# Kernel tuning notes

Measured on AMD Instinct MI355X. Metric: run time of the kernel, lower is better.

The kernel has to match this reference:

```python
import jax, jax.numpy as jnp
import numpy as np

NUM_HEADS = 8
MASK_RATE = 0.5


def setup_inputs() -> dict:
    key = jax.random.key(0)
    ks = jax.random.split(key, 6)
    B, N, C = 8, 1024, 256
    TABLE = 10
    att_embedding = jax.random.normal(ks[0], (B, N, C), dtype=jnp.float32)
    relation_position = jax.random.randint(ks[1], (B, N, N), 0, TABLE, dtype=jnp.int32)
    rel_len = jax.random.randint(ks[2], (B,), 0, 20, dtype=jnp.int32)
    W_qkv = jax.random.normal(ks[3], (C, 3 * C), dtype=jnp.float32) * (1.0 / np.sqrt(C))
    W_proj = jax.random.normal(ks[4], (C, C), dtype=jnp.float32) * (1.0 / np.sqrt(C))
    b_proj = jnp.zeros((C,), dtype=jnp.float32)
    bias_table = jax.random.normal(ks[5], (TABLE, NUM_HEADS), dtype=jnp.float32) * 0.02
    return {
        "att_embedding": att_embedding,
        "relation_position": relation_position,
        "rel_len": rel_len,
        "W_qkv": W_qkv,
        "W_proj": W_proj,
        "b_proj": b_proj,
        "bias_table": bias_table,
    }


def reference(att_embedding, relation_position, rel_len, W_qkv, W_proj, b_proj, bias_table):
    B, N, C = att_embedding.shape
    H = NUM_HEADS
    hd = C // H
    scale = hd ** -0.5

    # QKV projection (no bias): [B,N,3C] -> q,k,v each [B,H,N,hd]
    qkv = (att_embedding @ W_qkv).reshape(B, N, 3, H, hd)
    qkv = jnp.transpose(qkv, (2, 0, 3, 1, 4))
    q, k, v = qkv[0], qkv[1], qkv[2]

    # Attention scores [B,H,N,N]
    attn = jnp.einsum("bhnd,bhmd->bhnm", q, k) * scale

    # Relative position bias: gather [B,N,N,H] -> [B,H,N,N]
    pos_bias = jnp.transpose(bias_table[relation_position], (0, 3, 1, 2))

    # Mask bias: table row t gets -100 iff t > mask_len (mask_len+1 .. TABLE-1);
    # identical across heads -> compute as [B,1,N,N] instead of materializing [B,H,N,N].
    mask_len = (rel_len.astype(jnp.float32) * MASK_RATE).astype(jnp.int32)
    mask_bias = jnp.where(relation_position > mask_len[:, None, None], -100.0, 0.0)[:, None]

    attn = jax.nn.softmax(attn + pos_bias + mask_bias, axis=-1)

    # Weighted values -> [B,N,C] -> output projection
    x = jnp.einsum("bhnm,bhmd->bnhd", attn, v).reshape(B, N, C)
    x = x @ W_proj + b_proj
    return x
```

## Files before the change

kernel.cpp:

```cpp
#include <hip/hip_runtime.h>
#include <hip/hip_bf16.h>

typedef __bf16 bf16;
typedef __bf16 bf16x2 __attribute__((ext_vector_type(2)));
typedef __bf16 bf16x4 __attribute__((ext_vector_type(4)));
typedef __bf16 bf16x8 __attribute__((ext_vector_type(8)));
typedef float f32x4 __attribute__((ext_vector_type(4)));
typedef int i32x4 __attribute__((ext_vector_type(4)));

#define B_ 8
#define N_ 1024
#define C_ 256
#define H_ 8
#define C3_ 768
#define SCALE 0.17677669529663689f
#define FMAX 16.0f


__global__ __launch_bounds__(256) void gemm_qkv(
    const float* __restrict__ A, const float* __restrict__ Wqkv,
    const float* __restrict__ Wproj, const int* __restrict__ rel,
    bf16* __restrict__ q, bf16* __restrict__ kT, bf16* __restrict__ vT,
    bf16* __restrict__ Wp_tiled, unsigned char* __restrict__ rel8)
{
  __shared__ __align__(16) char sm[18432];

  int bb = blockIdx.x;
  int tid = threadIdx.x;

  if (bb >= 768) {
    if (bb < 2816) {
      long p = ((long)(bb - 768) * 256 + tid) * 16;
      i32x4 a = *reinterpret_cast<const i32x4*>(rel + p);
      i32x4 b2 = *reinterpret_cast<const i32x4*>(rel + p + 4);
      i32x4 c = *reinterpret_cast<const i32x4*>(rel + p + 8);
      i32x4 d = *reinterpret_cast<const i32x4*>(rel + p + 12);
      unsigned o0 = (unsigned)a[0] | ((unsigned)a[1] << 8) | ((unsigned)a[2] << 16) | ((unsigned)a[3] << 24);
      unsigned o1 = (unsigned)b2[0] | ((unsigned)b2[1] << 8) | ((unsigned)b2[2] << 16) | ((unsigned)b2[3] << 24);
      unsigned o2 = (unsigned)c[0] | ((unsigned)c[1] << 8) | ((unsigned)c[2] << 16) | ((unsigned)c[3] << 24);
      unsigned o3 = (unsigned)d[0] | ((unsigned)d[1] << 8) | ((unsigned)d[2] << 16) | ((unsigned)d[3] << 24);
      i32x4 ov = {(int)o0, (int)o1, (int)o2, (int)o3};
      *reinterpret_cast<i32x4*>(rel8 + p) = ov;
    } else {
      int p = (bb - 2816) * 256 + tid;
      int kk = p & 31;
      int n = (p >> 5) & 255;
      int kt = p >> 13;
      Wp_tiled[p] = (bf16)Wproj[(kt * 32 + kk) * C_ + n];
    }
    return;
  }

  bf16 (*As)[40] = (bf16(*)[40])(void*)sm;
  bf16 (*Bs)[40] = (bf16(*)[40])(void*)(sm + 5120);

  int wave = tid >> 6, lane = tid & 63, quad = lane >> 4, l16 = lane & 15;
  int x = bb & 127, y = bb >> 7;
  int m0 = x * 64, n0 = y * 128;
  int msub = (wave & 1) * 32, nsub = (wave >> 1) * 64;

  f32x4 acc[2][4] = {};

  int arow = tid >> 2, akc = (tid & 3) * 8;
  const float* aptr = A + (long)(m0 + arow) * C_ + akc;

  int bk = tid >> 3, bns = (tid & 7) * 16;
  int bcp = (((bk >> 3) ^ (tid & 3)) << 3) + (bk & 7);
  const float* wq = Wqkv + (long)bk * C3_ + n0 + bns;

  float4 a0 = *reinterpret_cast<const float4*>(aptr);
  float4 a1 = *reinterpret_cast<const float4*>(aptr + 4);
  float4 f0 = *reinterpret_cast<const float4*>(wq);
  float4 f1 = *reinterpret_cast<const float4*>(wq + 4);
  float4 f2 = *reinterpret_cast<const float4*>(wq + 8);
  float4 f3 = *reinterpret_cast<const float4*>(wq + 12);

  for (int kt = 0; kt < 8; ++kt) {
    __syncthreads();
    {
      bf16 at[8] = {(bf16)a0.x, (bf16)a0.y, (bf16)a0.z, (bf16)a0.w,
                    (bf16)a1.x, (bf16)a1.y, (bf16)a1.z, (bf16)a1.w};
      *reinterpret_cast<bf16x8*>(&As[arow][akc]) = *reinterpret_cast<bf16x8*>(at);
      float vv[16] = {f0.x, f0.y, f0.z, f0.w, f1.x, f1.y, f1.z, f1.w,
                      f2.x, f2.y, f2.z, f2.w, f3.x, f3.y, f3.z, f3.w};
#pragma unroll
      for (int i = 0; i < 16; ++i)
        Bs[bns + i][bcp] = (bf16)vv[i];
    }
    __syncthreads();

    if (kt < 7) {
      int kn = (kt + 1) * 32;
      a0 = *reinterpret_cast<const float4*>(aptr + kn);
      a1 = *reinterpret_cast<const float4*>(aptr + kn + 4);
      const float* wqn = wq + (long)kn * C3_;
      f0 = *reinterpret_cast<const float4*>(wqn);
      f1 = *reinterpret_cast<const float4*>(wqn + 4);
      f2 = *reinterpret_cast<const float4*>(wqn + 8);
      f3 = *reinterpret_cast<const float4*>(wqn + 12);
    }

    bf16x8 af[2], bfr[4];
#pragma unroll
    for (int mi = 0; mi < 2; ++mi)
      af[mi] = *reinterpret_cast<const bf16x8*>(&As[msub + mi * 16 + l16][quad * 8]);
#pragma unroll
    for (int ni = 0; ni < 4; ++ni)
      bfr[ni] = *reinterpret_cast<const bf16x8*>(
          &Bs[nsub + ni * 16 + l16][(quad ^ ni) << 3]);
#pragma unroll
    for (int mi = 0; mi < 2; ++mi)
#pragma unroll
      for (int ni = 0; ni < 4; ++ni)
        acc[mi][ni] = __builtin_amdgcn_mfma_f32_16x16x32_bf16(af[mi], bfr[ni], acc[mi][ni], 0, 0, 0);
  }

  __syncthreads();

  if (y < 4) {
    float mul = (y < 2) ? SCALE : 1.0f;
    bf16 (*Ep)[136] = (bf16(*)[136])(void*)sm;
#pragma unroll
    for (int mi = 0; mi < 2; ++mi)
#pragma unroll
      for (int ni = 0; ni < 4; ++ni)
#pragma unroll
        for (int r = 0; r < 4; ++r)
          Ep[msub + mi * 16 + quad * 4 + r][nsub + ni * 16 + l16] =
              (bf16)(acc[mi][ni][r] * mul);
    __syncthreads();
    int row = tid >> 2, seg = tid & 3;
    i32x4 w0 = *reinterpret_cast<const i32x4*>(&Ep[row][seg * 32]);
    i32x4 w1 = *reinterpret_cast<const i32x4*>(&Ep[row][seg * 32 + 8]);
    i32x4 w2 = *reinterpret_cast<const i32x4*>(&Ep[row][seg * 32 + 16]);
    i32x4 w3 = *reinterpret_cast<const i32x4*>(&Ep[row][seg * 32 + 24]);
    bf16* dst;
    if (y < 2) {
      dst = q + (long)(m0 + row) * 256 + n0 + seg * 32;
    } else {
      int c = n0 - 256 + seg * 32;
      int h = c >> 5;
      int gr = m0 + row, b = gr >> 10, n = gr & 1023;
      dst = kT + (((long)(b * H_ + h)) * N_ + n) * 32;
    }
    *reinterpret_cast<i32x4*>(dst) = w0;
    *reinterpret_cast<i32x4*>(dst + 8) = w1;
    *reinterpret_cast<i32x4*>(dst + 16) = w2;
    *reinterpret_cast<i32x4*>(dst + 24) = w3;
  } else {
    bf16 (*Vls)[72] = (bf16(*)[72])(void*)sm;
#pragma unroll
    for (int mi = 0; mi < 2; ++mi)
#pragma unroll
      for (int ni = 0; ni < 4; ++ni)
#pragma unroll
        for (int r = 0; r < 4; ++r) {
          int nn = msub + mi * 16 + quad * 4 + r;
          int np = (nn & ~31) | ((nn & 12) << 1) | (nn & 3) | (((nn >> 4) & 1) << 2);
          Vls[nsub + ni * 16 + l16][np] = (bf16)acc[mi][ni][r];
        }
    __syncthreads();
    int c = tid >> 1, nseg = (tid & 1) * 32;
    i32x4 w0 = *reinterpret_cast<const i32x4*>(&Vls[c][nseg]);
    i32x4 w1 = *reinterpret_cast<const i32x4*>(&Vls[c][nseg + 8]);
    i32x4 w2 = *reinterpret_cast<const i32x4*>(&Vls[c][nseg + 16]);
    i32x4 w3 = *reinterpret_cast<const i32x4*>(&Vls[c][nseg + 24]);
    int gb = m0 >> 10, mn = m0 & 1023;
    bf16* dst = vT + ((long)(gb * C_ + (n0 - 512) + c)) * N_ + mn + nseg;
    *reinterpret_cast<i32x4*>(dst) = w0;
    *reinterpret_cast<i32x4*>(dst + 8) = w1;
    *reinterpret_cast<i32x4*>(dst + 16) = w2;
    *reinterpret_cast<i32x4*>(dst + 24) = w3;
  }
}

__global__ __launch_bounds__(512) void flash_attn(
    const bf16* __restrict__ q, const bf16* __restrict__ kT,
    const bf16* __restrict__ vT, const unsigned char* __restrict__ rel8,
    const int* __restrict__ rel_len, const float* __restrict__ btab,
    const bf16* __restrict__ Wp_tiled, const float* __restrict__ bias,
    float* __restrict__ out)
{
  __shared__ __align__(16) char smem[74240];
  char* const KB0 = smem;
  char* const VB0 = smem + 32768;
  char* const RB0 = smem + 65536;
  float* const ebtl = (float*)(smem + 73728);

  int tid = threadIdx.x;
  int h = tid >> 6, lane = tid & 63, quad = lane >> 4, l16 = lane & 15;

  int wg = blockIdx.y * 64 + blockIdx.x;
  int swz = (wg & 7) * 64 + (wg >> 3);
  int b = swz >> 6, i0 = (swz & 63) * 16;
  long bN = (long)b * N_;

  int mask_len = (int)((float)rel_len[b] * 0.5f);
  if (tid < 80) {
    int t = tid >> 3, hh = tid & 7;
    ebtl[hh * 16 + t] = __expf(btab[t * H_ + hh] + (t > mask_len ? -100.f : 0.f) - FMAX);
  }

  bf16x8 qf = *reinterpret_cast<const bf16x8*>(
      q + (bN + i0 + l16) * 256 + h * 32 + quad * 8);

  __syncthreads();

  int l = lane;
  int sxc = (((l & 3) ^ ((l >> 3) & 3)) << 4);
  int kc0 = (l >> 2) * 64 + sxc;
  int vc0 = (h * 32 + (l >> 2)) * 2048 + sxc;
  int rc0 = (l >> 3) * 1024 + (l & 7) * 4;

  const char* kTb = (const char*)kT + ((long)(b * 8 + h) << 16);
  const char* vTb = (const char*)vT + (long)b * 524288;
  const char* rb8 = (const char*)rel8 + (bN + i0) * 1024;

  int swq = ((quad ^ ((l16 >> 1) & 3)) << 4);
  int kr = h * 2048 + l16 * 64 + swq;
  int rr = h * 512 + l16 * 32 + quad * 4;

#define KB(i) (KB0 + (i) * 16384)
#define VB(i) (VB0 + (i) * 16384)
#define RB(i) (RB0 + (i) * 4096)

#define GLD16(G, L) __builtin_amdgcn_global_load_lds(                         \
    (const __attribute__((address_space(1))) void*)(G),                       \
    (__attribute__((address_space(3))) void*)(L), 16, 0, 0)
#define GLD4(G, L) __builtin_amdgcn_global_load_lds(                          \
    (const __attribute__((address_space(1))) void*)(G),                       \
    (__attribute__((address_space(3))) void*)(L), 4, 0, 0)

#define GATH(G, RV0, RV1) do {                                                \
    _Pragma("unroll")                                                         \
    for (int e = 0; e < 4; ++e) {                                             \
      G[e]     = ebtl[h * 16 + (int)((RV0 >> (8 * e)) & 255u)];               \
      G[4 + e] = ebtl[h * 16 + (int)((RV1 >> (8 * e)) & 255u)];               \
    }                                                                         \
  } while (0)

#define COMP(K0, K1, V0, V1, G) do {                                          \
    f32x4 z = {};                                                             \
    f32x4 s0 = __builtin_amdgcn_mfma_f32_16x16x32_bf16(K0, qf, z, 0, 0, 0);   \
    f32x4 s1 = __builtin_amdgcn_mfma_f32_16x16x32_bf16(K1, qf, z, 0, 0, 0);   \
    bf16x8 pa;                                                                \
    _Pragma("unroll")                                                         \
    for (int e = 0; e < 4; ++e) {                                             \
      float p0 = __expf(s0[e]) * G[e];                                        \
      float p1 = __expf(s1[e]) * G[4 + e];                                    \
      l_acc += p0 + p1;                                                       \
      pa[e] = (bf16)p0;                                                       \
      pa[4 + e] = (bf16)p1;                                                   \
    }                                                                         \
    oacc[0] = __builtin_amdgcn_mfma_f32_16x16x32_bf16(pa, V0, oacc[0], 0, 0, 0); \
    oacc[1] = __builtin_amdgcn_mfma_f32_16x16x32_bf16(pa, V1, oacc[1], 0, 0, 0); \
  } while (0)

#define TILE(T_, KVR, KVW, GC, GN) do {                                       \
    int tn_ = ((T_) + 1) & 31, tr_ = ((T_) + 2) & 31;                         \
    GLD16(kTb + tn_ * 2048 + kc0,        KB(KVW) + h * 2048);                 \
    GLD16(kTb + tn_ * 2048 + kc0 + 1024, KB(KVW) + h * 2048 + 1024);          \
    GLD16(vTb + tn_ * 64 + vc0,          VB(KVW) + h * 2048);                 \
    GLD16(vTb + tn_ * 64 + vc0 + 32768,  VB(KVW) + h * 2048 + 1024);          \
    GLD4(rb8 + tr_ * 32 + rc0,           RB(KVR) + h * 512);                  \
    GLD4(rb8 + tr_ * 32 + rc0 + 8192,    RB(KVR) + h * 512 + 256);            \
    asm volatile("s_waitcnt vmcnt(6)" ::: "memory");                          \
    bf16x8 kf0 = *(const bf16x8*)(KB(KVR) + kr);                              \
    bf16x8 kf1 = *(const bf16x8*)(KB(KVR) + kr + 1024);                       \
    bf16x8 vf0 = *(const bf16x8*)(VB(KVR) + kr);                              \
    bf16x8 vf1 = *(const bf16x8*)(VB(KVR) + kr + 1024);                       \
    unsigned rv0 = *(const unsigned*)(RB(KVW) + rr);                          \
    unsigned rv1 = *(const unsigned*)(RB(KVW) + rr + 16);                     \
    GATH(GN, rv0, rv1);                                                       \
    COMP(kf0, kf1, vf0, vf1, GC);                                             \
  } while (0)

  f32x4 oacc[2] = {};
  float l_acc = 0.f;
  float gA[8], gB[8];

  GLD16(kTb + kc0,        KB(0) + h * 2048);
  GLD16(kTb + kc0 + 1024, KB(0) + h * 2048 + 1024);
  GLD16(vTb + vc0,          VB(0) + h * 2048);
  GLD16(vTb + vc0 + 32768,  VB(0) + h * 2048 + 1024);
  GLD4(rb8 + rc0,             RB(0) + h * 512);
  GLD4(rb8 + rc0 + 8192,      RB(0) + h * 512 + 256);
  GLD4(rb8 + 32 + rc0,        RB(1) + h * 512);
  GLD4(rb8 + 32 + rc0 + 8192, RB(1) + h * 512 + 256);
  asm volatile("s_waitcnt vmcnt(0)" ::: "memory");
  {
    unsigned rv0 = *(const unsigned*)(RB(0) + rr);
    unsigned rv1 = *(const unsigned*)(RB(0) + rr + 16);
    GATH(gA, rv0, rv1);
  }

#pragma unroll 1
  for (int t = 0; t < 32; t += 2) {
    TILE(t + 0, 0, 1, gA, gB);
    TILE(t + 1, 1, 0, gB, gA);
  }
#undef TILE
#undef COMP
#undef GATH
#undef GLD16
#undef GLD4
#undef KB
#undef VB
#undef RB

  asm volatile("s_waitcnt vmcnt(0)" ::: "memory");
  __syncthreads();

  float lsum = l_acc;
  lsum += __shfl_xor(lsum, 16);
  lsum += __shfl_xor(lsum, 32);
  float inv = 1.f / lsum;

  bf16 (*attL)[264] = (bf16(*)[264])(void*)smem;
#pragma unroll
  for (int r = 0; r < 4; ++r) {
    float invr = __shfl(inv, quad * 4 + r);
    attL[quad * 4 + r][h * 32 + l16] = (bf16)(oacc[0][r] * invr);
    attL[quad * 4 + r][h * 32 + 16 + l16] = (bf16)(oacc[1][r] * invr);
  }
  __syncthreads();

  f32x4 pacc[2] = {};
  const bf16* wp = Wp_tiled + ((h * 32 + l16) * 32 + quad * 8);
#pragma unroll
  for (int kt = 0; kt < 8; ++kt) {
    bf16x8 afr = *reinterpret_cast<const bf16x8*>(&attL[l16][kt * 32 + quad * 8]);
    bf16x8 b0 = *reinterpret_cast<const bf16x8*>(wp + kt * 8192);
    bf16x8 b1 = *reinterpret_cast<const bf16x8*>(wp + kt * 8192 + 512);
    pacc[0] = __builtin_amdgcn_mfma_f32_16x16x32_bf16(afr, b0, pacc[0], 0, 0, 0);
    pacc[1] = __builtin_amdgcn_mfma_f32_16x16x32_bf16(afr, b1, pacc[1], 0, 0, 0);
  }
  float bi0 = bias[h * 32 + l16];
  float bi1 = bias[h * 32 + 16 + l16];
#pragma unroll
  for (int r = 0; r < 4; ++r) {
    long rowoff = (bN + i0 + quad * 4 + r) * C_ + h * 32;
    out[rowoff + l16] = pacc[0][r] + bi0;
    out[rowoff + 16 + l16] = pacc[1][r] + bi1;
  }
}

extern "C" void kernel_launch(void* const* d_in, const int* in_sizes, int n_in,
                              void* d_out, int out_size, void* d_ws, size_t ws_size,
                              hipStream_t stream) {
  const float* X     = (const float*)d_in[0];
  const int*   rel   = (const int*)d_in[1];
  const int*   rlen  = (const int*)d_in[2];
  const float* Wqkv  = (const float*)d_in[3];
  const float* Wproj = (const float*)d_in[4];
  const float* bproj = (const float*)d_in[5];
  const float* btab  = (const float*)d_in[6];
  float* out = (float*)d_out;

  char* ws = (char*)d_ws;
  bf16* Wp_tiled = (bf16*)(ws + 393216);
  bf16* q  = (bf16*)(ws + 524288);
  bf16* kT = (bf16*)(ws + 524288 + 4194304);
  bf16* vT = (bf16*)(ws + 524288 + 2 * 4194304);
  unsigned char* rel8 = (unsigned char*)(ws + 13107200);

  gemm_qkv<<<dim3(3072), 256, 0, stream>>>(X, Wqkv, Wproj, rel,
                                           q, kT, vT, Wp_tiled, rel8);
  flash_attn<<<dim3(N_ / 16, B_), 512, 0, stream>>>(
      q, kT, vT, rel8, rlen, btab, Wp_tiled, bproj, out);
}
```

Measured before the change: 141.0 us.

## Process 32 query rows per block to reuse K/V tiles across two row groups

Each flash-attention workgroup now handles 32 query rows (two 16-row MFMA groups) instead of 16, so every K/V tile staged in LDS feeds twice as many MFMAs. The goal is to halve global K/V traffic per query. The grid halves to 256 blocks, the rel8 buffer doubles and its loads widen to 16 bytes, and register pressure rises. Fewer blocks may leave CUs underused on a 256-CU part.

Measured after the change: 131.3 us (median of 2 runs). 6.9% less time.

```diff
diff --git a/kernel.cpp b/kernel.cpp
--- a/kernel.cpp
+++ b/kernel.cpp
@@ -181,18 +181,18 @@
     const bf16* __restrict__ Wp_tiled, const float* __restrict__ bias,
     float* __restrict__ out)
 {
-  __shared__ __align__(16) char smem[74240];
+  __shared__ __align__(16) char smem[82432];
   char* const KB0 = smem;
   char* const VB0 = smem + 32768;
   char* const RB0 = smem + 65536;
-  float* const ebtl = (float*)(smem + 73728);
+  float* const ebtl = (float*)(smem + 81920);
 
   int tid = threadIdx.x;
   int h = tid >> 6, lane = tid & 63, quad = lane >> 4, l16 = lane & 15;
 
-  int wg = blockIdx.y * 64 + blockIdx.x;
-  int swz = (wg & 7) * 64 + (wg >> 3);
-  int b = swz >> 6, i0 = (swz & 63) * 16;
+  int wg = blockIdx.y * 32 + blockIdx.x;
+  int swz = (wg & 7) * 32 + (wg >> 3);
+  int b = swz >> 5, i0 = (swz & 31) * 32;
   long bN = (long)b * N_;
 
   int mask_len = (int)((float)rel_len[b] * 0.5f);
@@ -201,8 +201,10 @@
     ebtl[hh * 16 + t] = __expf(btab[t * H_ + hh] + (t > mask_len ? -100.f : 0.f) - FMAX);
   }
 
-  bf16x8 qf = *reinterpret_cast<const bf16x8*>(
+  bf16x8 qfA = *reinterpret_cast<const bf16x8*>(
       q + (bN + i0 + l16) * 256 + h * 32 + quad * 8);
+  bf16x8 qfB = *reinterpret_cast<const bf16x8*>(
+      q + (bN + i0 + 16 + l16) * 256 + h * 32 + quad * 8);
 
   __syncthreads();
 
@@ -210,7 +212,7 @@
   int sxc = (((l & 3) ^ ((l >> 3) & 3)) << 4);
   int kc0 = (l >> 2) * 64 + sxc;
   int vc0 = (h * 32 + (l >> 2)) * 2048 + sxc;
-  int rc0 = (l >> 3) * 1024 + (l & 7) * 4;
+  int rc0 = (l >> 1) * 1024 + (l & 1) * 16;
 
   const char* kTb = (const char*)kT + ((long)(b * 8 + h) << 16);
   const char* vTb = (const char*)vT + (long)b * 524288;
@@ -218,42 +220,48 @@
 
   int swq = ((quad ^ ((l16 >> 1) & 3)) << 4);
   int kr = h * 2048 + l16 * 64 + swq;
-  int rr = h * 512 + l16 * 32 + quad * 4;
+  int rr = h * 1024 + l16 * 32 + quad * 4;
 
 #define KB(i) (KB0 + (i) * 16384)
 #define VB(i) (VB0 + (i) * 16384)
-#define RB(i) (RB0 + (i) * 4096)
+#define RB(i) (RB0 + (i) * 8192)
 
 #define GLD16(G, L) __builtin_amdgcn_global_load_lds(                         \
     (const __attribute__((address_space(1))) void*)(G),                       \
     (__attribute__((address_space(3))) void*)(L), 16, 0, 0)
-#define GLD4(G, L) __builtin_amdgcn_global_load_lds(                          \
-    (const __attribute__((address_space(1))) void*)(G),                       \
-    (__attribute__((address_space(3))) void*)(L), 4, 0, 0)
-
-#define GATH(G, RV0, RV1) do {                                                \
+
+#define GATH(G, RV0, RV1, RV2, RV3) do {                                      \
     _Pragma("unroll")                                                         \
     for (int e = 0; e < 4; ++e) {                                             \
-      G[e]     = ebtl[h * 16 + (int)((RV0 >> (8 * e)) & 255u)];               \
-      G[4 + e] = ebtl[h * 16 + (int)((RV1 >> (8 * e)) & 255u)];               \
+      G[e]      = ebtl[h * 16 + (int)((RV0 >> (8 * e)) & 255u)];              \
+      G[4 + e]  = ebtl[h * 16 + (int)((RV1 >> (8 * e)) & 255u)];              \
+      G[8 + e]  = ebtl[h * 16 + (int)((RV2 >> (8 * e)) & 255u)];              \
+      G[12 + e] = ebtl[h * 16 + (int)((RV3 >> (8 * e)) & 255u)];              \
     }                                                                         \
   } while (0)
 
 #define COMP(K0, K1, V0, V1, G) do {                                          \
     f32x4 z = {};                                                             \
-    f32x4 s0 = __builtin_amdgcn_mfma_f32_16x16x32_bf16(K0, qf, z, 0, 0, 0);   \
-    f32x4 s1 = __builtin_amdgcn_mfma_f32_16x16x32_bf16(K1, qf, z, 0, 0, 0);   \
-    bf16x8 pa;                                                                \
+    f32x4 s0A = __builtin_amdgcn_mfma_f32_16x16x32_bf16(K0, qfA, z, 0, 0, 0); \
+    f32x4 s1A = __builtin_amdgcn_mfma_f32_16x16x32_bf16(K1, qfA, z, 0, 0, 0); \
+    f32x4 s0B = __builtin_amdgcn_mfma_f32_16x16x32_bf16(K0, qfB, z, 0, 0, 0); \
+    f32x4 s1B = __builtin_amdgcn_mfma_f32_16x16x32_bf16(K1, qfB, z, 0, 0, 0); \
+    bf16x8 paA, paB;                                                          \
     _Pragma("unroll")                                                         \
     for (int e = 0; e < 4; ++e) {                                             \
-      float p0 = __expf(s0[e]) * G[e];                                        \
-      float p1 = __expf(s1[e]) * G[4 + e];                                    \
-      l_acc += p0 + p1;                                                       \
-      pa[e] = (bf16)p0;                                                       \
-      pa[4 + e] = (bf16)p1;                                                   \
+      float pA0 = __expf(s0A[e]) * G[e];                                      \
+      float pA1 = __expf(s1A[e]) * G[4 + e];                                  \
+      float pB0 = __expf(s0B[e]) * G[8 + e];                                  \
+      float pB1 = __expf(s1B[e]) * G[12 + e];                                 \
+      l_accA += pA0 + pA1;                                                    \
+      l_accB += pB0 + pB1;                                                    \
+      paA[e] = (bf16)pA0; paA[4 + e] = (bf16)pA1;                             \
+      paB[e] = (bf16)pB0; paB[4 + e] = (bf16)pB1;                             \
     }                                                                         \
-    oacc[0] = __builtin_amdgcn_mfma_f32_16x16x32_bf16(pa, V0, oacc[0], 0, 0, 0); \
-    oacc[1] = __builtin_amdgcn_mfma_f32_16x16x32_bf16(pa, V1, oacc[1], 0, 0, 0); \
+    oA0 = __builtin_amdgcn_mfma_f32_16x16x32_bf16(paA, V0, oA0, 0, 0, 0);     \
+    oA1 = __builtin_amdgcn_mfma_f32_16x16x32_bf16(paA, V1, oA1, 0, 0, 0);     \
+    oB0 = __builtin_amdgcn_mfma_f32_16x16x32_bf16(paB, V0, oB0, 0, 0, 0);     \
+    oB1 = __builtin_amdgcn_mfma_f32_16x16x32_bf16(paB, V1, oB1, 0, 0, 0);     \
   } while (0)
 
 #define TILE(T_, KVR, KVW, GC, GN) do {                                       \
@@ -262,36 +270,37 @@
     GLD16(kTb + tn_ * 2048 + kc0 + 1024, KB(KVW) + h * 2048 + 1024);          \
     GLD16(vTb + tn_ * 64 + vc0,          VB(KVW) + h * 2048);                 \
     GLD16(vTb + tn_ * 64 + vc0 + 32768,  VB(KVW) + h * 2048 + 1024);          \
-    GLD4(rb8 + tr_ * 32 + rc0,           RB(KVR) + h * 512);                  \
-    GLD4(rb8 + tr_ * 32 + rc0 + 8192,    RB(KVR) + h * 512 + 256);            \
-    asm volatile("s_waitcnt vmcnt(6)" ::: "memory");                          \
+    GLD16(rb8 + tr_ * 32 + rc0,          RB(KVR) + h * 1024);                 \
+    asm volatile("s_waitcnt vmcnt(5)" ::: "memory");                          \
     bf16x8 kf0 = *(const bf16x8*)(KB(KVR) + kr);                              \
     bf16x8 kf1 = *(const bf16x8*)(KB(KVR) + kr + 1024);                       \
     bf16x8 vf0 = *(const bf16x8*)(VB(KVR) + kr);                              \
     bf16x8 vf1 = *(const bf16x8*)(VB(KVR) + kr + 1024);                       \
     unsigned rv0 = *(const unsigned*)(RB(KVW) + rr);                          \
     unsigned rv1 = *(const unsigned*)(RB(KVW) + rr + 16);                     \
-    GATH(GN, rv0, rv1);                                                       \
+    unsigned rv2 = *(const unsigned*)(RB(KVW) + rr + 512);                    \
+    unsigned rv3 = *(const unsigned*)(RB(KVW) + rr + 528);                    \
+    GATH(GN, rv0, rv1, rv2, rv3);                                             \
     COMP(kf0, kf1, vf0, vf1, GC);                                             \
   } while (0)
 
-  f32x4 oacc[2] = {};
-  float l_acc = 0.f;
-  float gA[8], gB[8];
+  f32x4 oA0 = {}, oA1 = {}, oB0 = {}, oB1 = {};
+  float l_accA = 0.f, l_accB = 0.f;
+  float gA[16], gB[16];
 
   GLD16(kTb + kc0,        KB(0) + h * 2048);
   GLD16(kTb + kc0 + 1024, KB(0) + h * 2048 + 1024);
   GLD16(vTb + vc0,          VB(0) + h * 2048);
   GLD16(vTb + vc0 + 32768,  VB(0) + h * 2048 + 1024);
-  GLD4(rb8 + rc0,             RB(0) + h * 512);
-  GLD4(rb8 + rc0 + 8192,      RB(0) + h * 512 + 256);
-  GLD4(rb8 + 32 + rc0,        RB(1) + h * 512);
-  GLD4(rb8 + 32 + rc0 + 8192, RB(1) + h * 512 + 256);
+  GLD16(rb8 + rc0,        RB(0) + h * 1024);
+  GLD16(rb8 + 32 + rc0,   RB(1) + h * 1024);
   asm volatile("s_waitcnt vmcnt(0)" ::: "memory");
   {
     unsigned rv0 = *(const unsigned*)(RB(0) + rr);
     unsigned rv1 = *(const unsigned*)(RB(0) + rr + 16);
-    GATH(gA, rv0, rv1);
+    unsigned rv2 = *(const unsigned*)(RB(0) + rr + 512);
+    unsigned rv3 = *(const unsigned*)(RB(0) + rr + 528);
+    GATH(gA, rv0, rv1, rv2, rv3);
   }
 
 #pragma unroll 1
@@ -303,7 +312,6 @@
 #undef COMP
 #undef GATH
 #undef GLD16
-#undef GLD4
 #undef KB
 #undef VB
 #undef RB
@@ -311,37 +319,50 @@
   asm volatile("s_waitcnt vmcnt(0)" ::: "memory");
   __syncthreads();
 
-  float lsum = l_acc;
-  lsum += __shfl_xor(lsum, 16);
-  lsum += __shfl_xor(lsum, 32);
-  float inv = 1.f / lsum;
+  float lsumA = l_accA;
+  lsumA += __shfl_xor(lsumA, 16);
+  lsumA += __shfl_xor(lsumA, 32);
+  float invA = 1.f / lsumA;
+  float lsumB = l_accB;
+  lsumB += __shfl_xor(lsumB, 16);
+  lsumB += __shfl_xor(lsumB, 32);
+  float invB = 1.f / lsumB;
 
   bf16 (*attL)[264] = (bf16(*)[264])(void*)smem;
 #pragma unroll
   for (int r = 0; r < 4; ++r) {
-    float invr = __shfl(inv, quad * 4 + r);
-    attL[quad * 4 + r][h * 32 + l16] = (bf16)(oacc[0][r] * invr);
-    attL[quad * 4 + r][h * 32 + 16 + l16] = (bf16)(oacc[1][r] * invr);
+    float invAr = __shfl(invA, quad * 4 + r);
+    float invBr = __shfl(invB, quad * 4 + r);
+    attL[quad * 4 + r][h * 32 + l16] = (bf16)(oA0[r] * invAr);
+    attL[quad * 4 + r][h * 32 + 16 + l16] = (bf16)(oA1[r] * invAr);
+    attL[16 + quad * 4 + r][h * 32 + l16] = (bf16)(oB0[r] * invBr);
+    attL[16 + quad * 4 + r][h * 32 + 16 + l16] = (bf16)(oB1[r] * invBr);
   }
   __syncthreads();
 
-  f32x4 pacc[2] = {};
+  f32x4 pA[2] = {}, pB[2] = {};
   const bf16* wp = Wp_tiled + ((h * 32 + l16) * 32 + quad * 8);
 #pragma unroll
   for (int kt = 0; kt < 8; ++kt) {
-    bf16x8 afr = *reinterpret_cast<const bf16x8*>(&attL[l16][kt * 32 + quad * 8]);
+    bf16x8 af0 = *reinterpret_cast<const bf16x8*>(&attL[l16][kt * 32 + quad * 8]);
+    bf16x8 af1 = *reinterpret_cast<const bf16x8*>(&attL[16 + l16][kt * 32 + quad * 8]);
     bf16x8 b0 = *reinterpret_cast<const bf16x8*>(wp + kt * 8192);
     bf16x8 b1 = *reinterpret_cast<const bf16x8*>(wp + kt * 8192 + 512);
-    pacc[0] = __builtin_amdgcn_mfma_f32_16x16x32_bf16(afr, b0, pacc[0], 0, 0, 0);
-    pacc[1] = __builtin_amdgcn_mfma_f32_16x16x32_bf16(afr, b1, pacc[1], 0, 0, 0);
+    pA[0] = __builtin_amdgcn_mfma_f32_16x16x32_bf16(af0, b0, pA[0], 0, 0, 0);
+    pA[1] = __builtin_amdgcn_mfma_f32_16x16x32_bf16(af0, b1, pA[1], 0, 0, 0);
+    pB[0] = __builtin_amdgcn_mfma_f32_16x16x32_bf16(af1, b0, pB[0], 0, 0, 0);
+    pB[1] = __builtin_amdgcn_mfma_f32_16x16x32_bf16(af1, b1, pB[1], 0, 0, 0);
   }
   float bi0 = bias[h * 32 + l16];
   float bi1 = bias[h * 32 + 16 + l16];
 #pragma unroll
   for (int r = 0; r < 4; ++r) {
-    long rowoff = (bN + i0 + quad * 4 + r) * C_ + h * 32;
-    out[rowoff + l16] = pacc[0][r] + bi0;
-    out[rowoff + 16 + l16] = pacc[1][r] + bi1;
+    long rowoffA = (bN + i0 + quad * 4 + r) * C_ + h * 32;
+    long rowoffB = (bN + i0 + 16 + quad * 4 + r) * C_ + h * 32;
+    out[rowoffA + l16] = pA[0][r] + bi0;
+    out[rowoffA + 16 + l16] = pA[1][r] + bi1;
+    out[rowoffB + l16] = pB[0][r] + bi0;
+    out[rowoffB + 16 + l16] = pB[1][r] + bi1;
   }
 }
 
@@ -366,6 +387,6 @@
 
   gemm_qkv<<<dim3(3072), 256, 0, stream>>>(X, Wqkv, Wproj, rel,
                                            q, kT, vT, Wp_tiled, rel8);
-  flash_attn<<<dim3(N_ / 16, B_), 512, 0, stream>>>(
+  flash_attn<<<dim3(32, B_), 512, 0, stream>>>(
       q, kT, vT, rel8, rlen, btab, Wp_tiled, bproj, out);
 }
```
